# Performance work log

Measured on AMD Instinct MI355X. Metric: run time of the kernel, lower is better.

The kernel has to match this reference:

```python
import jax, jax.numpy as jnp
import numpy as np
import math


def sinusoidal_embedding(n_pos, d_model, dtype=jnp.float32):
    # matches SpaceEmbedding: se[:,0::2]=sin(pos*div), se[:,1::2]=cos(pos*div)
    pos = jnp.arange(n_pos, dtype=dtype)[:, None]                      # [T,1]
    div = jnp.exp(jnp.arange(0, d_model, 2, dtype=dtype) * (-math.log(10000.0) / d_model))  # [d/2]
    ang = pos * div                                                    # [T,d/2]
    se = jnp.stack([jnp.sin(ang), jnp.cos(ang)], axis=-1).reshape(n_pos, d_model)
    return se


def setup_inputs() -> dict:
    key = jax.random.key(0)
    ks = jax.random.split(key, 6)
    B, D_in, T, d = 32, 512, 1024, 1024
    s_in = 1.0 / np.sqrt(D_in)
    s_d = 1.0 / np.sqrt(d)
    return {
        "xs": jax.random.normal(ks[0], (B, D_in, T), dtype=jnp.float32),
        "W_embed": jax.random.uniform(ks[1], (d, D_in), minval=-s_in, maxval=s_in, dtype=jnp.float32),
        "W_KQ": jax.random.uniform(ks[2], (d, d), minval=-s_d, maxval=s_d, dtype=jnp.float32),
        "W_PV": jax.random.uniform(ks[3], (d, d), minval=-s_d, maxval=s_d, dtype=jnp.float32),
        "W_un": jax.random.uniform(ks[4], (D_in, d), minval=-s_d, maxval=s_d, dtype=jnp.float32),
        "b_un": jnp.zeros((D_in,), dtype=jnp.float32),
    }


def reference(xs, W_embed, W_KQ, W_PV, W_un, b_un):
    B, D_in, T = xs.shape
    d = W_embed.shape[0]
    rho = 1.0
    # patch embedding: Linear(dim_input, d_model, bias=False) on [B,T,D_in]
    patch = jnp.einsum('bnt,dn->btd', xs, W_embed)                     # [B,T,d]
    emb = patch + sinusoidal_embedding(T, d, patch.dtype)[None]        # [B,T,d]
    E = jnp.transpose(emb, (0, 2, 1))                                  # [B,d,T]
    X = E[:, :, :-1]                                                   # [B,d,T-1] (skip last token)
    # attn_arg = X^T @ W_KQ @ E / rho  -> [B,T-1,T]
    attn_arg = jnp.einsum('bdm,de,bet->bmt', X, W_KQ, E) / rho
    soft = jax.nn.softmax(attn_arg, axis=1)                            # softmax over T-1 (keys) dim
    # f_attn = W_PV @ X @ soft -> [B,d,T]
    f_attn = jnp.einsum('de,bem,bmt->bdt', W_PV, X, soft)
    # unembed: Linear(d_model, dim_input) applied to [B,T,d], then transpose back
    out_full = jnp.einsum('bdt,od->bot', f_attn, W_un) + b_un[None, :, None]  # [B,D_in,T]
    return out_full, attn_arg
```

## Files before the change

kernel.cpp:

```cpp
#include <hip/hip_runtime.h>
#include <hip/hip_bf16.h>
#include <cstdio>

typedef __bf16 bf16;
typedef __bf16 bf16x4 __attribute__((ext_vector_type(4)));
typedef __bf16 bf16x8 __attribute__((ext_vector_type(8)));
typedef float  f32x4  __attribute__((ext_vector_type(4)));

#define AS1 __attribute__((address_space(1)))
#define AS3 __attribute__((address_space(3)))

__device__ __forceinline__ void async16(void* lds, const void* g) {
    __builtin_amdgcn_global_load_lds((AS1 unsigned int*)g, (AS3 unsigned int*)lds, 16, 0, 0);
}

enum { EPI_NONE = 0, EPI_SINUS = 1, EPI_BIAS = 2 };

#define FENCE asm volatile("" ::: "memory")
#define BAR   do { FENCE; __builtin_amdgcn_s_barrier(); FENCE; } while (0)
#define LGKM0 do { asm volatile("s_waitcnt lgkmcnt(0)" ::: "memory"); \
                   __builtin_amdgcn_sched_barrier(0); } while (0)
#define RD8(p) (*(const bf16x8*)(const void*)(p))

#define QUAD_MFMA(MB, NB)                                                      \
    _Pragma("unroll") for (int mf = 0; mf < 4; ++mf)                           \
    _Pragma("unroll") for (int nf = 0; nf < 2; ++nf)                           \
    _Pragma("unroll") for (int s = 0; s < 2; ++s)                              \
        acc[(MB) + mf][(NB) + nf] = __builtin_amdgcn_mfma_f32_16x16x32_bf16(   \
            af[(MB) + mf][s], bfr[(NB) + nf][s], acc[(MB) + mf][(NB) + nf], 0, 0, 0);

template <int EPI, typename CT>
__launch_bounds__(512, 2)
__global__ void gemm8(const bf16* __restrict__ A, long sA, int lda,
                      const bf16* __restrict__ B, long sB, int ldb,
                      CT* __restrict__ C, long sC, int ldc,
                      int K, int mLimit, const float* __restrict__ bias,
                      int tilesM, int tilesN)
{
    __shared__ __align__(16) char smem[131072];
    char* ldsA = smem;
    char* ldsB = smem + 65536;

    const int tid  = threadIdx.x;
    const int wave = tid >> 6;
    const int lane = tid & 63;
    const int quad = lane >> 4;
    const int l16  = lane & 15;
    const int hw   = wave >> 2;
    const int wq   = wave & 3;
    const int hbB  = wq >> 1;
    const int rrB  = (wq & 1) * 64;

    const int nwg = gridDim.x;
    const int qq = nwg >> 3, rr = nwg & 7;
    const int xcd = blockIdx.x & 7, idx = blockIdx.x >> 3;
    const int wgid = (xcd < rr ? xcd * (qq + 1) : rr * (qq + 1) + (xcd - rr) * qq) + idx;

    const int tpb = tilesM * tilesN;
    const int b   = wgid / tpb;
    const int rem = wgid - b * tpb;
    const int m0  = (rem / tilesN) * 256;
    const int n0  = (rem % tilesN) * 256;

    A += (long)b * sA;
    B += (long)b * sB;

    const int odt  = wave * 1024 + lane * 16;
    const int ol   = odt ^ (((odt >> 7) & 7) << 4);
    const int srow = ol >> 7;
    const int scol = (ol & 127) >> 1;
    const bf16* pA = A + (long)(m0 + srow) * lda + scol;
    const bf16* pB = B + (long)(n0 + srow) * ldb + scol;

    const int xr = (l16 & 7) << 4;
    const int lane2_0 = ((l16 * 128) + (quad * 16)) ^ xr;
    const int lane2_1 = ((l16 * 128) + 64 + (quad * 16)) ^ xr;

    auto stgA = [&](int bb, int h, int kt) {
        char* l = ldsA + bb * 32768 + h * 16384 + wave * 1024;
        const bf16* g = pA + (long)(h * 128) * lda + kt * 64;
        async16(l, g);
        async16(l + 8192, g + (long)64 * lda);
    };
    auto stgB = [&](int bb, int h, int kt) {
        char* l = ldsB + bb * 32768 + h * 16384 + wave * 1024;
        const bf16* g = pB + (long)(h * 128) * ldb + kt * 64;
        async16(l, g);
        async16(l + 8192, g + (long)64 * ldb);
    };

    const int nk = K >> 6;

    stgA(0, 0, 0); stgA(0, 1, 0);
    stgB(0, 0, 0); stgB(0, 1, 0);
    stgA(1, 0, 1); stgA(1, 1, 1);
    asm volatile("s_waitcnt vmcnt(4)" ::: "memory");
    BAR;

    bf16x8 af[8][2], bfr[4][2];
    f32x4 acc[8][4] = {};

    for (int t = 0; t < nk; ++t) {
        const int cur = t & 1;
        const char* aH = ldsA + cur * 32768 + hw * 16384;
        const char* bH = ldsB + cur * 32768 + hbB * 16384 + rrB * 128;

        #pragma unroll
        for (int mf = 0; mf < 4; ++mf) {
            af[mf][0] = RD8(aH + mf * 2048 + lane2_0);
            af[mf][1] = RD8(aH + mf * 2048 + lane2_1);
        }
        #pragma unroll
        for (int nf = 0; nf < 2; ++nf) {
            bfr[nf][0] = RD8(bH + nf * 2048 + lane2_0);
            bfr[nf][1] = RD8(bH + nf * 2048 + lane2_1);
        }
        if (t + 1 < nk) stgB(cur ^ 1, 0, t + 1);
        BAR;
        LGKM0;
        __builtin_amdgcn_s_setprio(1);
        QUAD_MFMA(0, 0);
        __builtin_amdgcn_s_setprio(0);
        BAR;

        #pragma unroll
        for (int mf = 4; mf < 8; ++mf) {
            af[mf][0] = RD8(aH + mf * 2048 + lane2_0);
            af[mf][1] = RD8(aH + mf * 2048 + lane2_1);
        }
        if (t + 1 < nk) stgB(cur ^ 1, 1, t + 1);
        BAR;
        LGKM0;
        __builtin_amdgcn_s_setprio(1);
        QUAD_MFMA(4, 0);
        __builtin_amdgcn_s_setprio(0);
        BAR;

        #pragma unroll
        for (int nf = 2; nf < 4; ++nf) {
            bfr[nf][0] = RD8(bH + nf * 2048 + lane2_0);
            bfr[nf][1] = RD8(bH + nf * 2048 + lane2_1);
        }
        if (t + 2 < nk) stgA(cur, 0, t + 2);
        BAR;
        LGKM0;
        __builtin_amdgcn_s_setprio(1);
        QUAD_MFMA(4, 2);
        __builtin_amdgcn_s_setprio(0);
        BAR;

        if (t + 2 < nk) {
            stgA(cur, 1, t + 2);
            asm volatile("s_waitcnt vmcnt(4)" ::: "memory");
        } else {
            asm volatile("s_waitcnt vmcnt(0)" ::: "memory");
        }
        BAR;
        __builtin_amdgcn_s_setprio(1);
        QUAD_MFMA(0, 2);
        __builtin_amdgcn_s_setprio(0);
        BAR;
    }

    C += (long)b * sC;

    #pragma unroll
    for (int nf = 0; nf < 4; ++nf) {
        const int col = n0 + wq * 64 + nf * 16 + l16;
        float fr = 0.f;
        if (EPI == EPI_SINUS)
            fr = __expf((float)(-(col & ~1)) * (9.210340371976184f / 1024.f));
        #pragma unroll
        for (int mf = 0; mf < 8; ++mf) {
            #pragma unroll
            for (int r = 0; r < 4; ++r) {
                const int row = m0 + hw * 128 + mf * 16 + quad * 4 + r;
                float v = acc[mf][nf][r];
                if (EPI == EPI_SINUS) {
                    float ang = (float)row * fr;
                    v += (col & 1) ? __cosf(ang) : __sinf(ang);
                }
                if (EPI == EPI_BIAS) v += bias[row];
                if (row < mLimit)
                    C[(long)row * ldc + col] = (CT)v;
            }
        }
    }
}

__launch_bounds__(256)
__global__ void cvt_f32_bf16(const float* __restrict__ in, bf16* __restrict__ out, int n)
{
    int i = (blockIdx.x * 256 + threadIdx.x) * 4;
    if (i < n) {
        float4 v = *(const float4*)(in + i);
        out[i]     = (bf16)v.x;
        out[i + 1] = (bf16)v.y;
        out[i + 2] = (bf16)v.z;
        out[i + 3] = (bf16)v.w;
    }
}

__launch_bounds__(256)
__global__ void transpose_f32_bf16(const float* __restrict__ in, bf16* __restrict__ out,
                                   int rows, int cols)
{
    __shared__ float tile[32][33];
    const long bs = (long)rows * cols;
    in  += (long)blockIdx.z * bs;
    out += (long)blockIdx.z * bs;
    const int c0 = blockIdx.x * 32, r0 = blockIdx.y * 32;
    const int tx = threadIdx.x, ty = threadIdx.y;
    #pragma unroll
    for (int i = ty; i < 32; i += 8)
        tile[i][tx] = in[(long)(r0 + i) * cols + c0 + tx];
    __syncthreads();
    #pragma unroll
    for (int i = ty; i < 32; i += 8)
        out[(long)(c0 + i) * rows + r0 + tx] = (bf16)tile[tx][i];
}

__launch_bounds__(256)
__global__ void transpose_bf16(const bf16* __restrict__ in, bf16* __restrict__ out,
                               int rows, int cols)
{
    __shared__ bf16 tile[32][33];
    const long bs = (long)rows * cols;
    in  += (long)blockIdx.z * bs;
    out += (long)blockIdx.z * bs;
    const int c0 = blockIdx.x * 32, r0 = blockIdx.y * 32;
    const int tx = threadIdx.x, ty = threadIdx.y;
    #pragma unroll
    for (int i = ty; i < 32; i += 8)
        tile[i][tx] = in[(long)(r0 + i) * cols + c0 + tx];
    __syncthreads();
    #pragma unroll
    for (int i = ty; i < 32; i += 8)
        out[(long)(c0 + i) * rows + r0 + tx] = tile[tx][i];
}

__device__ __forceinline__ void onl_upd(float v, float& mx, float& sm) {
    if (v > mx) { sm = sm * __expf(mx - v) + 1.f; mx = v; }
    else        { sm += __expf(v - mx); }
}

__device__ __forceinline__ void onl_merge(float& mx, float& sm, float omx, float osm) {
    float nm = fmaxf(mx, omx);
    sm = sm * __expf(mx - nm) + osm * __expf(omx - nm);
    mx = nm;
}

__launch_bounds__(256)
__global__ void softmax_part(const float* __restrict__ attn,
                             float* __restrict__ pmx, float* __restrict__ psum)
{
    const int b   = blockIdx.z, mt = blockIdx.y;
    const int c   = threadIdx.x & 63;
    const int g   = threadIdx.x >> 6;
    const int col = blockIdx.x * 256 + c * 4;
    const float* a = attn + (long)b * (1023l * 1024) + col;

    const int m0   = mt * 128;
    const int mEnd = (m0 + 128 < 1023) ? m0 + 128 : 1023;

    float4 mx = make_float4(-1e30f, -1e30f, -1e30f, -1e30f);
    float4 sm = make_float4(0.f, 0.f, 0.f, 0.f);
    for (int m = m0 + g; m < mEnd; m += 4) {
        float4 v = *(const float4*)(a + (long)m * 1024);
        onl_upd(v.x, mx.x, sm.x); onl_upd(v.y, mx.y, sm.y);
        onl_upd(v.z, mx.z, sm.z); onl_upd(v.w, mx.w, sm.w);
    }

    __shared__ float4 lmx[4][64], lsm[4][64];
    lmx[g][c] = mx; lsm[g][c] = sm;
    __syncthreads();
    if (g == 0) {
        float4 MX = lmx[0][c], SM = lsm[0][c];
        #pragma unroll
        for (int gg = 1; gg < 4; gg++) {
            float4 omx = lmx[gg][c], osm = lsm[gg][c];
            onl_merge(MX.x, SM.x, omx.x, osm.x);
            onl_merge(MX.y, SM.y, omx.y, osm.y);
            onl_merge(MX.z, SM.z, omx.z, osm.z);
            onl_merge(MX.w, SM.w, omx.w, osm.w);
        }
        const long po = ((long)b * 8 + mt) * 1024 + col;
        *(float4*)(pmx + po)  = MX;
        *(float4*)(psum + po) = SM;
    }
}

__launch_bounds__(256)
__global__ void softmax_norm(const float* __restrict__ attn,
                             const float* __restrict__ pmx,
                             const float* __restrict__ psum,
                             bf16* __restrict__ soft)
{
    const int b   = blockIdx.z, mt = blockIdx.y;
    const int c   = threadIdx.x & 63;
    const int g   = threadIdx.x >> 6;
    const int col = blockIdx.x * 256 + c * 4;
    const float* a = attn + (long)b * (1023l * 1024) + col;
    bf16* s        = soft + (long)b * (1024l * 1024) + col;

    float4 MX = make_float4(-1e30f, -1e30f, -1e30f, -1e30f);
    float4 SM = make_float4(0.f, 0.f, 0.f, 0.f);
    #pragma unroll
    for (int t = 0; t < 8; t++) {
        const long po = ((long)b * 8 + t) * 1024 + col;
        float4 omx = *(const float4*)(pmx + po);
        float4 osm = *(const float4*)(psum + po);
        onl_merge(MX.x, SM.x, omx.x, osm.x);
        onl_merge(MX.y, SM.y, omx.y, osm.y);
        onl_merge(MX.z, SM.z, omx.z, osm.z);
        onl_merge(MX.w, SM.w, omx.w, osm.w);
    }
    const float4 INV = make_float4(1.f / SM.x, 1.f / SM.y, 1.f / SM.z, 1.f / SM.w);

    const int m0   = mt * 128;
    const int mEnd = (m0 + 128 < 1023) ? m0 + 128 : 1023;
    for (int m = m0 + g; m < mEnd; m += 4) {
        float4 v = *(const float4*)(a + (long)m * 1024);
        bf16x4 o;
        o[0] = (bf16)(__expf(v.x - MX.x) * INV.x);
        o[1] = (bf16)(__expf(v.y - MX.y) * INV.y);
        o[2] = (bf16)(__expf(v.z - MX.z) * INV.z);
        o[3] = (bf16)(__expf(v.w - MX.w) * INV.w);
        *(bf16x4*)(s + (long)m * 1024) = o;
    }
    if (mt == 7 && g == 3) {
        bf16x4 z = {(bf16)0.f, (bf16)0.f, (bf16)0.f, (bf16)0.f};
        *(bf16x4*)(s + 1023l * 1024) = z;
    }
}

extern "C" void kernel_launch(void* const* d_in, const int* in_sizes, int n_in,
                              void* d_out, int out_size, void* d_ws, size_t ws_size,
                              hipStream_t stream)
{
    const float* xs    = (const float*)d_in[0];
    const float* W_emb = (const float*)d_in[1];
    const float* W_KQ  = (const float*)d_in[2];
    const float* W_PV  = (const float*)d_in[3];
    const float* W_un  = (const float*)d_in[4];
    const float* b_un  = (const float*)d_in[5];

    float* out  = (float*)d_out;
    float* attn = out + (size_t)32 * 512 * 1024;

    const long MB = 1024l * 1024;

    char* ws = (char*)d_ws;
    const size_t oXsT  = 0;
    const size_t oET   = oXsT + (size_t)33554432;
    const size_t oEn   = oET  + (size_t)67108864;
    const size_t oQT   = oEn  + (size_t)67108864;
    const size_t oR    = oQT  + (size_t)67108864;
    const size_t oWe   = oR   + (size_t)67108864;
    const size_t oWkq  = oWe  + (size_t)1048576;
    const size_t oWpv  = oWkq + (size_t)2097152;
    const size_t oWun  = oWpv + (size_t)2097152;
    const size_t need  = oWun + (size_t)1048576;
    if (ws_size < need) { fprintf(stderr, "ws too small: %zu < %zu\n", ws_size, need); return; }

    bf16* xsT   = (bf16*)(ws + oXsT);
    bf16* ET    = (bf16*)(ws + oET);
    bf16* En    = (bf16*)(ws + oEn);
    bf16* QT    = (bf16*)(ws + oQT);
    bf16* R     = (bf16*)(ws + oR);
    bf16* We    = (bf16*)(ws + oWe);
    bf16* Wkq   = (bf16*)(ws + oWkq);
    bf16* Wpv   = (bf16*)(ws + oWpv);
    bf16* Wun   = (bf16*)(ws + oWun);
    bf16* soft  = ET;
    bf16* softT = QT;
    bf16* A1T   = R;
    bf16* fT    = ET;

    float* pmx  = (float*)(ws + oR);
    float* psum = pmx + (size_t)32 * 8 * 1024;

    const dim3 tb(32, 8);
    const int BIG = 1 << 30;

    cvt_f32_bf16<<<512, 256, 0, stream>>>(W_emb, We, 524288);
    cvt_f32_bf16<<<1024, 256, 0, stream>>>(W_KQ, Wkq, 1048576);
    cvt_f32_bf16<<<1024, 256, 0, stream>>>(W_PV, Wpv, 1048576);
    cvt_f32_bf16<<<512, 256, 0, stream>>>(W_un, Wun, 524288);
    transpose_f32_bf16<<<dim3(32, 16, 32), tb, 0, stream>>>(xs, xsT, 512, 1024);
    gemm8<EPI_SINUS, bf16><<<dim3(512), 512, 0, stream>>>(
        xsT, 512l * 1024, 512, We, 0, 512, ET, MB, 1024, 512, BIG, nullptr, 4, 4);
    transpose_bf16<<<dim3(32, 32, 32), tb, 0, stream>>>(ET, En, 1024, 1024);
    gemm8<EPI_NONE, bf16><<<dim3(512), 512, 0, stream>>>(
        ET, MB, 1024, Wkq, 0, 1024, QT, MB, 1024, 1024, BIG, nullptr, 4, 4);
    gemm8<EPI_NONE, float><<<dim3(512), 512, 0, stream>>>(
        ET, MB, 1024, QT, MB, 1024, attn, 1023l * 1024, 1024, 1024, 1023, nullptr, 4, 4);
    softmax_part<<<dim3(4, 8, 32), 256, 0, stream>>>(attn, pmx, psum);
    softmax_norm<<<dim3(4, 8, 32), 256, 0, stream>>>(attn, pmx, psum, soft);
    transpose_bf16<<<dim3(32, 32, 32), tb, 0, stream>>>(soft, softT, 1024, 1024);
    gemm8<EPI_NONE, bf16><<<dim3(512), 512, 0, stream>>>(
        softT, MB, 1024, En, MB, 1024, A1T, MB, 1024, 1024, BIG, nullptr, 4, 4);
    gemm8<EPI_NONE, bf16><<<dim3(512), 512, 0, stream>>>(
        A1T, MB, 1024, Wpv, 0, 1024, fT, MB, 1024, 1024, BIG, nullptr, 4, 4);
    gemm8<EPI_BIAS, float><<<dim3(256), 512, 0, stream>>>(
        Wun, 0, 1024, fT, MB, 1024, out, 512l * 1024, 1024, 1024, BIG, b_un, 2, 4);
}
```

Baseline: 829.1 us.

## Fuse softmax partial stats into attn GEMM epilogue and merge normalize with transpose

The attention-score GEMM epilogue now computes per-column max and sum partials over its 256-row tile, using shuffles and an LDS reduction, and writes them out. This removes the separate softmax_part pass over the fp32 attention matrix. A new softmax_norm_T kernel normalizes and writes the transposed bf16 softmax directly, eliminating the separate soft buffer and transpose kernel. The GEMM main loop also reorders fragment loads so A/B fragments are split into per-phase arrays, which may lower register pressure. The cost is a heavier GEMM epilogue and a transposing normalize pass that reads fp32 one column per thread.

Measured after the change: 801.1 us. 1.03x faster.

```diff
diff --git a/kernel.cpp b/kernel.cpp
--- a/kernel.cpp
+++ b/kernel.cpp
@@ -14,7 +14,7 @@
     __builtin_amdgcn_global_load_lds((AS1 unsigned int*)g, (AS3 unsigned int*)lds, 16, 0, 0);
 }
 
-enum { EPI_NONE = 0, EPI_SINUS = 1, EPI_BIAS = 2 };
+enum { EPI_NONE = 0, EPI_SINUS = 1, EPI_BIAS = 2, EPI_ATTN = 3 };
 
 #define FENCE asm volatile("" ::: "memory")
 #define BAR   do { FENCE; __builtin_amdgcn_s_barrier(); FENCE; } while (0)
@@ -22,12 +22,18 @@
                    __builtin_amdgcn_sched_barrier(0); } while (0)
 #define RD8(p) (*(const bf16x8*)(const void*)(p))
 
-#define QUAD_MFMA(MB, NB)                                                      \
+#define MFMA_Q(AF, MB, BF, NB)                                                 \
     _Pragma("unroll") for (int mf = 0; mf < 4; ++mf)                           \
     _Pragma("unroll") for (int nf = 0; nf < 2; ++nf)                           \
     _Pragma("unroll") for (int s = 0; s < 2; ++s)                              \
         acc[(MB) + mf][(NB) + nf] = __builtin_amdgcn_mfma_f32_16x16x32_bf16(   \
-            af[(MB) + mf][s], bfr[(NB) + nf][s], acc[(MB) + mf][(NB) + nf], 0, 0, 0);
+            AF[mf][s], BF[nf][s], acc[(MB) + mf][(NB) + nf], 0, 0, 0);
+
+__device__ __forceinline__ void onl_merge(float& mx, float& sm, float omx, float osm) {
+    float nm = fmaxf(mx, omx);
+    sm = sm * __expf(mx - nm) + osm * __expf(omx - nm);
+    mx = nm;
+}
 
 template <int EPI, typename CT>
 __launch_bounds__(512, 2)
@@ -35,6 +41,7 @@
                       const bf16* __restrict__ B, long sB, int ldb,
                       CT* __restrict__ C, long sC, int ldc,
                       int K, int mLimit, const float* __restrict__ bias,
+                      float* __restrict__ pmx, float* __restrict__ psum,
                       int tilesM, int tilesN)
 {
     __shared__ __align__(16) char smem[131072];
@@ -97,7 +104,6 @@
     asm volatile("s_waitcnt vmcnt(4)" ::: "memory");
     BAR;
 
-    bf16x8 af[8][2], bfr[4][2];
     f32x4 acc[8][4] = {};
 
     for (int t = 0; t < nk; ++t) {
@@ -105,47 +111,49 @@
         const char* aH = ldsA + cur * 32768 + hw * 16384;
         const char* bH = ldsB + cur * 32768 + hbB * 16384 + rrB * 128;
 
+        bf16x8 af03[4][2], af47[4][2], bf01[2][2], bf23[2][2];
+
         #pragma unroll
         for (int mf = 0; mf < 4; ++mf) {
-            af[mf][0] = RD8(aH + mf * 2048 + lane2_0);
-            af[mf][1] = RD8(aH + mf * 2048 + lane2_1);
+            af03[mf][0] = RD8(aH + mf * 2048 + lane2_0);
+            af03[mf][1] = RD8(aH + mf * 2048 + lane2_1);
         }
         #pragma unroll
         for (int nf = 0; nf < 2; ++nf) {
-            bfr[nf][0] = RD8(bH + nf * 2048 + lane2_0);
-            bfr[nf][1] = RD8(bH + nf * 2048 + lane2_1);
+            bf01[nf][0] = RD8(bH + nf * 2048 + lane2_0);
+            bf01[nf][1] = RD8(bH + nf * 2048 + lane2_1);
         }
         if (t + 1 < nk) stgB(cur ^ 1, 0, t + 1);
         BAR;
         LGKM0;
         __builtin_amdgcn_s_setprio(1);
-        QUAD_MFMA(0, 0);
+        MFMA_Q(af03, 0, bf01, 0);
         __builtin_amdgcn_s_setprio(0);
         BAR;
 
         #pragma unroll
-        for (int mf = 4; mf < 8; ++mf) {
-            af[mf][0] = RD8(aH + mf * 2048 + lane2_0);
-            af[mf][1] = RD8(aH + mf * 2048 + lane2_1);
+        for (int nf = 0; nf < 2; ++nf) {
+            bf23[nf][0] = RD8(bH + (nf + 2) * 2048 + lane2_0);
+            bf23[nf][1] = RD8(bH + (nf + 2) * 2048 + lane2_1);
         }
         if (t + 1 < nk) stgB(cur ^ 1, 1, t + 1);
         BAR;
         LGKM0;
         __builtin_amdgcn_s_setprio(1);
-        QUAD_MFMA(4, 0);
+        MFMA_Q(af03, 0, bf23, 2);
         __builtin_amdgcn_s_setprio(0);
         BAR;
 
         #pragma unroll
-        for (int nf = 2; nf < 4; ++nf) {
-            bfr[nf][0] = RD8(bH + nf * 2048 + lane2_0);
-            bfr[nf][1] = RD8(bH + nf * 2048 + lane2_1);
+        for (int mf = 0; mf < 4; ++mf) {
+            af47[mf][0] = RD8(aH + (mf + 4) * 2048 + lane2_0);
+            af47[mf][1] = RD8(aH + (mf + 4) * 2048 + lane2_1);
         }
         if (t + 2 < nk) stgA(cur, 0, t + 2);
         BAR;
         LGKM0;
         __builtin_amdgcn_s_setprio(1);
-        QUAD_MFMA(4, 2);
+        MFMA_Q(af47, 4, bf01, 0);
         __builtin_amdgcn_s_setprio(0);
         BAR;
 
@@ -157,7 +165,7 @@
         }
         BAR;
         __builtin_amdgcn_s_setprio(1);
-        QUAD_MFMA(0, 2);
+        MFMA_Q(af47, 4, bf23, 2);
         __builtin_amdgcn_s_setprio(0);
         BAR;
     }
@@ -186,6 +194,50 @@
             }
         }
     }
+
+    if (EPI == EPI_ATTN) {
+        float nmx[4], nsm[4];
+        #pragma unroll
+        for (int nf = 0; nf < 4; ++nf) {
+            float mx = -1e30f;
+            #pragma unroll
+            for (int mf = 0; mf < 8; ++mf)
+                #pragma unroll
+                for (int r = 0; r < 4; ++r) {
+                    const int row = m0 + hw * 128 + mf * 16 + quad * 4 + r;
+                    float v = (row < mLimit) ? acc[mf][nf][r] : -1e30f;
+                    mx = fmaxf(mx, v);
+                }
+            float sm = 0.f;
+            #pragma unroll
+            for (int mf = 0; mf < 8; ++mf)
+                #pragma unroll
+                for (int r = 0; r < 4; ++r) {
+                    const int row = m0 + hw * 128 + mf * 16 + quad * 4 + r;
+                    float v = (row < mLimit) ? acc[mf][nf][r] : -1e30f;
+                    sm += __expf(v - mx);
+                }
+            float omx = __shfl_xor(mx, 16), osm = __shfl_xor(sm, 16);
+            onl_merge(mx, sm, omx, osm);
+            omx = __shfl_xor(mx, 32); osm = __shfl_xor(sm, 32);
+            onl_merge(mx, sm, omx, osm);
+            nmx[nf] = mx; nsm[nf] = sm;
+        }
+        float smx = quad == 0 ? nmx[0] : quad == 1 ? nmx[1] : quad == 2 ? nmx[2] : nmx[3];
+        float ssm = quad == 0 ? nsm[0] : quad == 1 ? nsm[1] : quad == 2 ? nsm[2] : nsm[3];
+        float2* red = (float2*)smem;
+        red[wave * 64 + lane] = make_float2(smx, ssm);
+        __syncthreads();
+        if (wave < 4) {
+            float2 x = red[wave * 64 + lane];
+            float2 y = red[(wave + 4) * 64 + lane];
+            onl_merge(x.x, x.y, y.x, y.y);
+            const int col = n0 + wq * 64 + lane;
+            const int mt  = m0 >> 8;
+            pmx [((long)b * 4 + mt) * 1024 + col] = x.x;
+            psum[((long)b * 4 + mt) * 1024 + col] = x.y;
+        }
+    }
 }
 
 __launch_bounds__(256)
@@ -239,99 +291,43 @@
         out[(long)(c0 + i) * rows + r0 + tx] = tile[tx][i];
 }
 
-__device__ __forceinline__ void onl_upd(float v, float& mx, float& sm) {
-    if (v > mx) { sm = sm * __expf(mx - v) + 1.f; mx = v; }
-    else        { sm += __expf(v - mx); }
-}
-
-__device__ __forceinline__ void onl_merge(float& mx, float& sm, float omx, float osm) {
-    float nm = fmaxf(mx, omx);
-    sm = sm * __expf(mx - nm) + osm * __expf(omx - nm);
-    mx = nm;
-}
-
 __launch_bounds__(256)
-__global__ void softmax_part(const float* __restrict__ attn,
-                             float* __restrict__ pmx, float* __restrict__ psum)
-{
-    const int b   = blockIdx.z, mt = blockIdx.y;
-    const int c   = threadIdx.x & 63;
-    const int g   = threadIdx.x >> 6;
-    const int col = blockIdx.x * 256 + c * 4;
-    const float* a = attn + (long)b * (1023l * 1024) + col;
-
-    const int m0   = mt * 128;
-    const int mEnd = (m0 + 128 < 1023) ? m0 + 128 : 1023;
-
-    float4 mx = make_float4(-1e30f, -1e30f, -1e30f, -1e30f);
-    float4 sm = make_float4(0.f, 0.f, 0.f, 0.f);
-    for (int m = m0 + g; m < mEnd; m += 4) {
-        float4 v = *(const float4*)(a + (long)m * 1024);
-        onl_upd(v.x, mx.x, sm.x); onl_upd(v.y, mx.y, sm.y);
-        onl_upd(v.z, mx.z, sm.z); onl_upd(v.w, mx.w, sm.w);
-    }
-
-    __shared__ float4 lmx[4][64], lsm[4][64];
-    lmx[g][c] = mx; lsm[g][c] = sm;
+__global__ void softmax_norm_T(const float* __restrict__ attn,
+                               const float* __restrict__ pmx,
+                               const float* __restrict__ psum,
+                               bf16* __restrict__ softT)
+{
+    __shared__ bf16 tile[64][66];
+    const int b  = blockIdx.z;
+    const int mt = blockIdx.x;
+    const int ct = blockIdx.y;
+    const int tx = threadIdx.x & 63;
+    const int ty = threadIdx.x >> 6;
+    const int col = ct * 64 + tx;
+
+    float MX = -1e30f, SM = 0.f;
+    #pragma unroll
+    for (int p = 0; p < 4; ++p) {
+        float omx = pmx [((long)b * 4 + p) * 1024 + col];
+        float osm = psum[((long)b * 4 + p) * 1024 + col];
+        onl_merge(MX, SM, omx, osm);
+    }
+    const float INV = 1.f / SM;
+
+    const float* a = attn + (long)b * (1023l * 1024);
+    const int m0 = mt * 64;
+    #pragma unroll
+    for (int i = ty; i < 64; i += 4) {
+        const int m = m0 + i;
+        float p = 0.f;
+        if (m < 1023) p = __expf(a[(long)m * 1024 + col] - MX) * INV;
+        tile[tx][i] = (bf16)p;
+    }
     __syncthreads();
-    if (g == 0) {
-        float4 MX = lmx[0][c], SM = lsm[0][c];
-        #pragma unroll
-        for (int gg = 1; gg < 4; gg++) {
-            float4 omx = lmx[gg][c], osm = lsm[gg][c];
-            onl_merge(MX.x, SM.x, omx.x, osm.x);
-            onl_merge(MX.y, SM.y, omx.y, osm.y);
-            onl_merge(MX.z, SM.z, omx.z, osm.z);
-            onl_merge(MX.w, SM.w, omx.w, osm.w);
-        }
-        const long po = ((long)b * 8 + mt) * 1024 + col;
-        *(float4*)(pmx + po)  = MX;
-        *(float4*)(psum + po) = SM;
-    }
-}
-
-__launch_bounds__(256)
-__global__ void softmax_norm(const float* __restrict__ attn,
-                             const float* __restrict__ pmx,
-                             const float* __restrict__ psum,
-                             bf16* __restrict__ soft)
-{
-    const int b   = blockIdx.z, mt = blockIdx.y;
-    const int c   = threadIdx.x & 63;
-    const int g   = threadIdx.x >> 6;
-    const int col = blockIdx.x * 256 + c * 4;
-    const float* a = attn + (long)b * (1023l * 1024) + col;
-    bf16* s        = soft + (long)b * (1024l * 1024) + col;
-
-    float4 MX = make_float4(-1e30f, -1e30f, -1e30f, -1e30f);
-    float4 SM = make_float4(0.f, 0.f, 0.f, 0.f);
-    #pragma unroll
-    for (int t = 0; t < 8; t++) {
-        const long po = ((long)b * 8 + t) * 1024 + col;
-        float4 omx = *(const float4*)(pmx + po);
-        float4 osm = *(const float4*)(psum + po);
-        onl_merge(MX.x, SM.x, omx.x, osm.x);
-        onl_merge(MX.y, SM.y, omx.y, osm.y);
-        onl_merge(MX.z, SM.z, omx.z, osm.z);
-        onl_merge(MX.w, SM.w, omx.w, osm.w);
-    }
-    const float4 INV = make_float4(1.f / SM.x, 1.f / SM.y, 1.f / SM.z, 1.f / SM.w);
-
-    const int m0   = mt * 128;
-    const int mEnd = (m0 + 128 < 1023) ? m0 + 128 : 1023;
-    for (int m = m0 + g; m < mEnd; m += 4) {
-        float4 v = *(const float4*)(a + (long)m * 1024);
-        bf16x4 o;
-        o[0] = (bf16)(__expf(v.x - MX.x) * INV.x);
-        o[1] = (bf16)(__expf(v.y - MX.y) * INV.y);
-        o[2] = (bf16)(__expf(v.z - MX.z) * INV.z);
-        o[3] = (bf16)(__expf(v.w - MX.w) * INV.w);
-        *(bf16x4*)(s + (long)m * 1024) = o;
-    }
-    if (mt == 7 && g == 3) {
-        bf16x4 z = {(bf16)0.f, (bf16)0.f, (bf16)0.f, (bf16)0.f};
-        *(bf16x4*)(s + 1023l * 1024) = z;
-    }
+    bf16* o = softT + (long)b * (1024l * 1024) + (long)(ct * 64) * 1024 + m0;
+    #pragma unroll
+    for (int j = ty; j < 64; j += 4)
+        o[(long)j * 1024 + tx] = tile[j][tx];
 }
 
 extern "C" void kernel_launch(void* const* d_in, const int* in_sizes, int n_in,
@@ -367,18 +363,16 @@
     bf16* ET    = (bf16*)(ws + oET);
     bf16* En    = (bf16*)(ws + oEn);
     bf16* QT    = (bf16*)(ws + oQT);
-    bf16* R     = (bf16*)(ws + oR);
     bf16* We    = (bf16*)(ws + oWe);
     bf16* Wkq   = (bf16*)(ws + oWkq);
     bf16* Wpv   = (bf16*)(ws + oWpv);
     bf16* Wun   = (bf16*)(ws + oWun);
-    bf16* soft  = ET;
     bf16* softT = QT;
-    bf16* A1T   = R;
+    bf16* A1T   = (bf16*)(ws + oR);
     bf16* fT    = ET;
 
     float* pmx  = (float*)(ws + oR);
-    float* psum = pmx + (size_t)32 * 8 * 1024;
+    float* psum = pmx + (size_t)32 * 4 * 1024;
 
     const dim3 tb(32, 8);
     const int BIG = 1 << 30;
@@ -389,19 +383,17 @@
     cvt_f32_bf16<<<512, 256, 0, stream>>>(W_un, Wun, 524288);
     transpose_f32_bf16<<<dim3(32, 16, 32), tb, 0, stream>>>(xs, xsT, 512, 1024);
     gemm8<EPI_SINUS, bf16><<<dim3(512), 512, 0, stream>>>(
-        xsT, 512l * 1024, 512, We, 0, 512, ET, MB, 1024, 512, BIG, nullptr, 4, 4);
+        xsT, 512l * 1024, 512, We, 0, 512, ET, MB, 1024, 512, BIG, nullptr, nullptr, nullptr, 4, 4);
     transpose_bf16<<<dim3(32, 32, 32), tb, 0, stream>>>(ET, En, 1024, 1024);
     gemm8<EPI_NONE, bf16><<<dim3(512), 512, 0, stream>>>(
-        ET, MB, 1024, Wkq, 0, 1024, QT, MB, 1024, 1024, BIG, nullptr, 4, 4);
-    gemm8<EPI_NONE, float><<<dim3(512), 512, 0, stream>>>(
-        ET, MB, 1024, QT, MB, 1024, attn, 1023l * 1024, 1024, 1024, 1023, nullptr, 4, 4);
-    softmax_part<<<dim3(4, 8, 32), 256, 0, stream>>>(attn, pmx, psum);
-    softmax_norm<<<dim3(4, 8, 32), 256, 0, stream>>>(attn, pmx, psum, soft);
-    transpose_bf16<<<dim3(32, 32, 32), tb, 0, stream>>>(soft, softT, 1024, 1024);
+        ET, MB, 1024, Wkq, 0, 1024, QT, MB, 1024, 1024, BIG, nullptr, nullptr, nullptr, 4, 4);
+    gemm8<EPI_ATTN, float><<<dim3(512), 512, 0, stream>>>(
+        ET, MB, 1024, QT, MB, 1024, attn, 1023l * 1024, 1024, 1024, 1023, nullptr, pmx, psum, 4, 4);
+    softmax_norm_T<<<dim3(16, 16, 32), 256, 0, stream>>>(attn, pmx, psum, softT);
     gemm8<EPI_NONE, bf16><<<dim3(512), 512, 0, stream>>>(
-        softT, MB, 1024, En, MB, 1024, A1T, MB, 1024, 1024, BIG, nullptr, 4, 4);
+        softT, MB, 1024, En, MB, 1024, A1T, MB, 1024, 1024, BIG, nullptr, nullptr, nullptr, 4, 4);
     gemm8<EPI_NONE, bf16><<<dim3(512), 512, 0, stream>>>(
-        A1T, MB, 1024, Wpv, 0, 1024, fT, MB, 1024, 1024, BIG, nullptr, 4, 4);
+        A1T, MB, 1024, Wpv, 0, 1024, fT, MB, 1024, 1024, BIG, nullptr, nullptr, nullptr, 4, 4);
     gemm8<EPI_BIAS, float><<<dim3(256), 512, 0, stream>>>(
-        Wun, 0, 1024, fT, MB, 1024, out, 512l * 1024, 1024, 1024, BIG, b_un, 2, 4);
-}
+        Wun, 0, 1024, fT, MB, 1024, out, 512l * 1024, 1024, 1024, BIG, b_un, nullptr, nullptr, 2, 4);
+}
```
